# Optimization experiments

Measured on AMD Instinct MI355X. Metric: run time of the kernel, lower is better.

The kernel has to match this reference:

```python
import jax, jax.numpy as jnp
import numpy as np

H = 64          # index_n_heads
D = 128         # index_head_dim (== FP8 quant block size -> one scale per row)
RD = 64         # qk_rope_head_dim
TOPK = 512      # index_topk
THETA = 10000.0
SM_SCALE = D ** -0.5


def _fwht(x):
    """Sylvester-ordered fast Walsh-Hadamard transform over last dim, scaled by d^-0.5."""
    d = x.shape[-1]
    orig = x.shape
    y = x.reshape(-1, d)
    m = 1
    while m < d:  # static loop, log2(d)=7 iters
        y = y.reshape(-1, d // (2 * m), 2, m)
        a, b = y[:, :, 0, :], y[:, :, 1, :]
        y = jnp.stack([a + b, a - b], axis=2)
        m *= 2
    return y.reshape(orig) * (d ** -0.5)


def _interleaved_to_half(x):
    # [..., d] with (even, odd) interleaving -> [evens..., odds...]
    return jnp.concatenate([x[..., 0::2], x[..., 1::2]], axis=-1)


def _rope_half(x, cos, sin):
    # x: [..., RD] in half format; cos/sin broadcastable to [..., RD//2]
    x1, x2 = x[..., : RD // 2], x[..., RD // 2:]
    return jnp.concatenate([x1 * cos - x2 * sin, x2 * cos + x1 * sin], axis=-1)


def _layernorm(x, g, b, eps=1e-5):
    mu = jnp.mean(x, axis=-1, keepdims=True)
    var = jnp.mean(jnp.square(x - mu), axis=-1, keepdims=True)
    return (x - mu) * jax.lax.rsqrt(var + eps) * g + b


def _fp8_ue8m0_quant(x2d):
    """Per-row FP8 e4m3 quantization with UE8M0 (power-of-two) scales. x2d: (M, 128)."""
    amax = jnp.maximum(jnp.max(jnp.abs(x2d), axis=1), 1e-4)
    sf = jnp.exp2(jnp.ceil(jnp.log2(amax / 448.0)))               # (M,)
    xq = (x2d * (1.0 / sf)[:, None]).astype(jnp.float8_e4m3fn)
    return xq, sf


def _indexer_fwd(hidden_states, q_lora, positions, wq_b, wk, w_proj, ln_gamma, ln_beta):
    T = hidden_states.shape[0]
    # --- projections ---
    q = (q_lora @ wq_b).reshape(T, H, D)                          # (T,H,D)
    k = _layernorm(hidden_states @ wk, ln_gamma, ln_beta)         # (T,D)
    # --- RoPE on leading RD dims (interleaved -> half, then half rotation) ---
    inv_freq = 1.0 / (THETA ** (jnp.arange(0, RD, 2, dtype=jnp.float32) / RD))  # (RD/2,)
    ang = positions.astype(jnp.float32)[:, None] * inv_freq       # (T,RD/2)
    cos, sin = jnp.cos(ang), jnp.sin(ang)
    q_rot = _rope_half(_interleaved_to_half(q[..., :RD]), cos[:, None, :], sin[:, None, :])
    k_rot = _rope_half(_interleaved_to_half(k[..., :RD]), cos, sin)
    q = jnp.concatenate([q_rot, q[..., RD:]], axis=-1)
    k = jnp.concatenate([k_rot, k[..., RD:]], axis=-1)
    # --- Hadamard rotation ---
    q = _fwht(q)
    k = _fwht(k)
    # --- FP8 UE8M0 quantization (head_dim == quant block -> 1 scale per row) ---
    q_fp8, q_scale = _fp8_ue8m0_quant(q.reshape(T * H, D))
    k_fp8, k_scale = _fp8_ue8m0_quant(k)
    q_scale = q_scale.reshape(T, H)
    # --- gate weights: weights_proj * H^-0.5 * q_scale * softmax_scale ---
    weights = (hidden_states @ w_proj) * (H ** -0.5) * q_scale * SM_SCALE  # (T,H)
    # --- MQA indexer scoring: dequant matmul, ReLU, head-weighted sum ---
    qd = q_fp8.astype(jnp.float32).reshape(T, H, D)
    kd = k_fp8.astype(jnp.float32) * k_scale[:, None]             # (T,D)
    logits = jnp.einsum('thd,sd->ths', qd, kd)                    # (T,H,S)
    scores = jnp.einsum('th,ths->ts', weights, jax.nn.relu(logits))  # (T,S)
    # --- causal mask + top-k token selection ---
    t_idx = jnp.arange(T)
    causal = t_idx[None, :] <= t_idx[:, None]                     # (T,S): s <= t
    scores = jnp.where(causal, scores, jnp.float32(-1e30))
    vals, idx = jax.lax.top_k(scores, TOPK)
    return vals, idx


def setup_inputs() -> dict:
    key = jax.random.key(0)
    ks = jax.random.split(key, 5)
    T, HID, R = 1024, 7168, 1536
    return {
        'hidden_states': jax.random.normal(ks[0], (T, HID), jnp.float32),
        'q_lora': jax.random.normal(ks[1], (T, R), jnp.float32),
        'positions': jnp.arange(T, dtype=jnp.int32),
        'wq_b': jax.random.normal(ks[2], (R, H * D), jnp.float32) * (R ** -0.5),
        'wk': jax.random.normal(ks[3], (HID, D), jnp.float32) * (HID ** -0.5),
        'w_proj': jax.random.normal(ks[4], (HID, H), jnp.float32) * (HID ** -0.5),
        'ln_gamma': jnp.ones((D,), jnp.float32),
        'ln_beta': jnp.zeros((D,), jnp.float32),
    }


def reference(hidden_states, q_lora, positions, wq_b, wk, w_proj, ln_gamma, ln_beta):
    return _indexer_fwd(hidden_states, q_lora, positions, wq_b, wk, w_proj, ln_gamma, ln_beta)
```

## Files before the change

kernel.cpp:

```cpp
#include <hip/hip_runtime.h>
#include <cstdint>
#include <cmath>

#define NT 1024
#define NHID 7168
#define NR 1536
#define NH 64
#define ND 128
#define NTOPK 512
#define TTILE 4
#define KSPLIT 16

typedef float f32x4 __attribute__((ext_vector_type(4)));
typedef ushort u16x8 __attribute__((ext_vector_type(8)));

__device__ __forceinline__ ushort f2bf(float x) {
  uint32_t u = __float_as_uint(x);
  u += 0x7fffu + ((u >> 16) & 1u);
  return (ushort)(u >> 16);
}
__device__ __forceinline__ float bf2f(ushort u) {
  return __uint_as_float(((uint32_t)u) << 16);
}
__device__ __forceinline__ void gload_lds16(const void* g, void* l) {
  __builtin_amdgcn_global_load_lds(
      (const __attribute__((address_space(1))) uint32_t*)g,
      (__attribute__((address_space(3))) uint32_t*)l, 16, 0, 0);
}
__device__ __forceinline__ uint32_t pk_fp8x4(float a, float b, float c, float d) {
  uint32_t lo = (uint32_t)__builtin_amdgcn_cvt_pk_fp8_f32(a, b, 0, false) & 0xffffu;
  uint32_t hi = (uint32_t)__builtin_amdgcn_cvt_pk_fp8_f32(c, d, 0, false) << 16;
  return lo | hi;
}

__global__ void rope_table_k(const int* __restrict__ pos,
                             float* __restrict__ cost, float* __restrict__ sint) {
  int i = threadIdx.x;
  int t = blockIdx.x;
  if (i < 32) {
    double x = (double)(2 * i) / 64.0;
    double p = pow(10000.0, x);
    float p32 = (float)p;
    float invf = __fdiv_rn(1.0f, p32);
    float ang = __fmul_rn((float)pos[t], invf);
    cost[t * 32 + i] = (float)cos((double)ang);
    sint[t * 32 + i] = (float)sin((double)ang);
  }
}

__global__ __launch_bounds__(256)
void cast_fp8_k(const float* __restrict__ in, uint32_t* __restrict__ out,
                int n8, float scale) {
  int i = blockIdx.x * 256 + threadIdx.x;
  if (i >= n8) return;
  const f32x4* p = (const f32x4*)(in + (size_t)i * 8);
  f32x4 a = p[0], b = p[1];
  out[(size_t)i * 2] =
      pk_fp8x4(a[0] * scale, a[1] * scale, a[2] * scale, a[3] * scale);
  out[(size_t)i * 2 + 1] =
      pk_fp8x4(b[0] * scale, b[1] * scale, b[2] * scale, b[3] * scale);
}

__global__ __launch_bounds__(256)
void tcast_fp8_k(const float* __restrict__ in, uint8_t* __restrict__ out,
                 int K, int N, float scale) {
  __shared__ uint8_t t8[64][68];
  int tid = threadIdx.x;
  int n0 = blockIdx.x * 64, k0 = blockIdx.y * 64;
  int r = tid >> 4, c = (tid & 15) * 4;
#pragma unroll
  for (int rr = 0; rr < 64; rr += 16) {
    f32x4 v = *(const f32x4*)(in + (size_t)(k0 + rr + r) * N + n0 + c);
    *(uint32_t*)&t8[rr + r][c] =
        pk_fp8x4(v[0] * scale, v[1] * scale, v[2] * scale, v[3] * scale);
  }
  __syncthreads();
#pragma unroll
  for (int rr = 0; rr < 64; rr += 16) {
    int orow = rr + r;
    uint32_t w = (uint32_t)t8[c + 0][orow] | ((uint32_t)t8[c + 1][orow] << 8) |
                 ((uint32_t)t8[c + 2][orow] << 16) | ((uint32_t)t8[c + 3][orow] << 24);
    *(uint32_t*)(out + (size_t)(n0 + orow) * K + k0 + c) = w;
  }
}

template <int BM, int BN, bool OUTBF>
__global__ __launch_bounds__(256)
void gemm_fp8_k(const uint8_t* __restrict__ A, const uint8_t* __restrict__ Bt,
                void* __restrict__ Cv, int M, int N, int K, int kchunk) {
  constexpr int FM = BM / 32;
  constexpr int FN = BN / 32;
  __shared__ uint8_t As[2 * BM * 64];
  __shared__ uint8_t Bs[2 * BN * 64];
  int tid = threadIdx.x;
  int wave = tid >> 6, lane = tid & 63;
  int ln = lane & 15, lg = lane >> 4;
  int n0 = blockIdx.x * BN, m0 = blockIdx.y * BM;
  int k0 = blockIdx.z * kchunk;
  int wm = (wave >> 1) * (BM / 2), wn = (wave & 1) * (BN / 2);

  f32x4 acc[FM][FN];
#pragma unroll
  for (int m = 0; m < FM; m++)
#pragma unroll
    for (int n = 0; n < FN; n++) acc[m][n] = {0.f, 0.f, 0.f, 0.f};

  auto stage = [&](int buf, int kk0) {
#pragma unroll
    for (int c = 0; c < BM / 64; c++) {
      int o = c * 256 + wave * 64 + lane;
      int row = o >> 2, g = o & 3;
      int gs = g ^ ((row >> 1) & 3);
      gload_lds16(A + (size_t)(m0 + row) * K + kk0 + gs * 16,
                  (char*)As + buf * (BM * 64) + o * 16);
    }
#pragma unroll
    for (int c = 0; c < BN / 64; c++) {
      int o = c * 256 + wave * 64 + lane;
      int row = o >> 2, g = o & 3;
      int gs = g ^ ((row >> 1) & 3);
      gload_lds16(Bt + (size_t)(n0 + row) * K + kk0 + gs * 16,
                  (char*)Bs + buf * (BN * 64) + o * 16);
    }
  };

  int ntile = kchunk / 64;
  stage(0, k0);
  __syncthreads();
  int cur = 0;
  for (int t = 0; t < ntile; t++) {
    if (t + 1 < ntile) stage(cur ^ 1, k0 + (t + 1) * 64);
    const uint8_t* ap = As + cur * (BM * 64);
    const uint8_t* bp = Bs + cur * (BN * 64);
#pragma unroll
    for (int kk = 0; kk < 2; kk++) {
      long af[FM], bfr[FN];
#pragma unroll
      for (int m = 0; m < FM; m++) {
        int row = wm + m * 16 + ln;
        int g = kk * 2 + (lg >> 1);
        int rd = row * 64 + ((g ^ ((row >> 1) & 3)) << 4) + (lg & 1) * 8;
        af[m] = *(const long*)(ap + rd);
      }
#pragma unroll
      for (int n = 0; n < FN; n++) {
        int row = wn + n * 16 + ln;
        int g = kk * 2 + (lg >> 1);
        int rd = row * 64 + ((g ^ ((row >> 1) & 3)) << 4) + (lg & 1) * 8;
        bfr[n] = *(const long*)(bp + rd);
      }
#pragma unroll
      for (int m = 0; m < FM; m++)
#pragma unroll
        for (int n = 0; n < FN; n++)
          acc[m][n] = __builtin_amdgcn_mfma_f32_16x16x32_fp8_fp8(af[m], bfr[n],
                                                                 acc[m][n], 0, 0, 0);
    }
    __syncthreads();
    cur ^= 1;
  }

  if constexpr (OUTBF) {
    ushort* Cb = (ushort*)Cv;
#pragma unroll
    for (int m = 0; m < FM; m++)
#pragma unroll
      for (int n = 0; n < FN; n++)
#pragma unroll
        for (int j = 0; j < 4; j++) {
          int row = m0 + wm + m * 16 + lg * 4 + j;
          int col = n0 + wn + n * 16 + ln;
          Cb[(size_t)row * N + col] = f2bf(acc[m][n][j]);
        }
  } else {
    float* C = (float*)Cv + (size_t)blockIdx.z * M * N;
#pragma unroll
    for (int m = 0; m < FM; m++)
#pragma unroll
      for (int n = 0; n < FN; n++)
#pragma unroll
        for (int j = 0; j < 4; j++) {
          int row = m0 + wm + m * 16 + lg * 4 + j;
          int col = n0 + wn + n * 16 + ln;
          C[(size_t)row * N + col] = acc[m][n][j];
        }
  }
}

__device__ __forceinline__ void rope_fwht_quant(
    float v0, float v1, int l, int pos_t,
    const float* __restrict__ cost, const float* __restrict__ sint,
    uint8_t* __restrict__ out_bytes, float* __restrict__ out_scale) {
  float a = __shfl(v0, (2 * l) & 63, 64);
  float b = __shfl(v0, (2 * l + 1) & 63, 64);
  int fi = l & 31;
  float c = cost[pos_t * 32 + fi];
  float sn = sint[pos_t * 32 + fi];
  float r;
  if (l < 32)
    r = __fsub_rn(__fmul_rn(a, c), __fmul_rn(b, sn));
  else
    r = __fadd_rn(__fmul_rn(b, c), __fmul_rn(a, sn));
  v0 = r;

#pragma unroll
  for (int m = 1; m < 64; m <<= 1) {
    float p0 = __shfl_xor(v0, m, 64);
    float p1 = __shfl_xor(v1, m, 64);
    bool up = (l & m) == 0;
    v0 = up ? __fadd_rn(v0, p0) : __fsub_rn(p0, v0);
    v1 = up ? __fadd_rn(v1, p1) : __fsub_rn(p1, v1);
  }
  {
    float A0 = v0, B0 = v1;
    v0 = __fadd_rn(A0, B0);
    v1 = __fsub_rn(A0, B0);
  }
  const float WS = 0.08838834764831843f;
  v0 = __fmul_rn(v0, WS);
  v1 = __fmul_rn(v1, WS);

  float am = fmaxf(fabsf(v0), fabsf(v1));
#pragma unroll
  for (int m = 1; m < 64; m <<= 1) am = fmaxf(am, __shfl_xor(am, m, 64));
  am = fmaxf(am, 1e-4f);
  float ratio = __fdiv_rn(am, 448.0f);
  uint32_t rb = __float_as_uint(ratio);
  int e = (int)((rb + 0x7fffffu) >> 23) - 127;
  float sf = __uint_as_float((uint32_t)(e + 127) << 23);
  float inv = __uint_as_float((uint32_t)(127 - e) << 23);
  float q0 = __fmul_rn(v0, inv);
  float q1 = __fmul_rn(v1, inv);
  int b0 = __builtin_amdgcn_cvt_pk_fp8_f32(q0, q0, 0, false);
  int b1 = __builtin_amdgcn_cvt_pk_fp8_f32(q1, q1, 0, false);
  out_bytes[l] = (uint8_t)(b0 & 0xff);
  out_bytes[l + 64] = (uint8_t)(b1 & 0xff);
  if (l == 0) *out_scale = sf;
}

__global__ __launch_bounds__(256)
void kfin_weights_k(const float* __restrict__ kpart, const float* __restrict__ gamma,
                    const float* __restrict__ beta, const float* __restrict__ cost,
                    const float* __restrict__ sint, const float* __restrict__ qscale,
                    uint8_t* __restrict__ kfp8, float* __restrict__ kscale,
                    float* __restrict__ weights) {
  int l = threadIdx.x & 63;
  int row = blockIdx.x * 4 + (threadIdx.x >> 6);
  float v0 = 0.0f, v1 = 0.0f, ws = 0.0f;
#pragma unroll
  for (int p = 0; p < KSPLIT; p++) {
    const float* base = kpart + (size_t)p * (NT * 192) + row * 192;
    v0 = __fadd_rn(v0, base[l]);
    v1 = __fadd_rn(v1, base[l + 64]);
    ws = __fadd_rn(ws, base[128 + l]);
  }
  float w = __fmul_rn(ws, 0.001953125f);
  w = __fmul_rn(w, qscale[row * NH + l]);
  w = __fmul_rn(w, 0.08838834764831843f);
  weights[row * NH + l] = w;
  float s = __fadd_rn(v0, v1);
#pragma unroll
  for (int m = 1; m < 64; m <<= 1) s = __fadd_rn(s, __shfl_xor(s, m, 64));
  float mu = __fmul_rn(s, 0.0078125f);
  float d0 = __fsub_rn(v0, mu), d1 = __fsub_rn(v1, mu);
  float vs = __fadd_rn(__fmul_rn(d0, d0), __fmul_rn(d1, d1));
#pragma unroll
  for (int m = 1; m < 64; m <<= 1) vs = __fadd_rn(vs, __shfl_xor(vs, m, 64));
  float var = __fmul_rn(vs, 0.0078125f);
  float rs = (float)(1.0 / sqrt((double)__fadd_rn(var, 1e-5f)));
  v0 = __fadd_rn(__fmul_rn(__fmul_rn(d0, rs), gamma[l]), beta[l]);
  v1 = __fadd_rn(__fmul_rn(__fmul_rn(d1, rs), gamma[l + 64]), beta[l + 64]);
  rope_fwht_quant(v0, v1, l, row, cost, sint, kfp8 + (size_t)row * ND, kscale + row);
}

__global__ __launch_bounds__(256)
void q_finalize_k(const ushort* __restrict__ qraw, const float* __restrict__ cost,
                  const float* __restrict__ sint, uint8_t* __restrict__ qfp8,
                  float* __restrict__ qscale) {
  int l = threadIdx.x & 63;
  int row = blockIdx.x * 4 + (threadIdx.x >> 6);
  int t = row >> 6;
  float v0 = bf2f(qraw[(size_t)row * ND + l]);
  float v1 = bf2f(qraw[(size_t)row * ND + l + 64]);
  rope_fwht_quant(v0, v1, l, t, cost, sint, qfp8 + (size_t)row * ND, qscale + row);
}

__global__ __launch_bounds__(256)
void scores_k(const uint8_t* __restrict__ qfp8, const uint8_t* __restrict__ kfp8,
              const float* __restrict__ weights, float* __restrict__ scores) {
  __shared__ uint8_t q_lds[TTILE * 64 * 128];
  __shared__ uint8_t k_lds[128 * 128];
  __shared__ float w_lds[TTILE * 64];

  int b = blockIdx.x;
  int g = 0;
  while (g < 7 && b >= 16 * (g + 1) * (g + 2)) g++;
  int r = b - 16 * g * (g + 1);
  int a = 32 * g + r / (g + 1);
  int chunk = r % (g + 1);
  int t0 = a * TTILE;
  int s0 = chunk * 128;

  int tid = threadIdx.x;
  int wave = tid >> 6, lane = tid & 63;
  int lg = lane >> 4, ln = lane & 15;

  const uint8_t* qbase = qfp8 + (size_t)t0 * 64 * 128;
#pragma unroll
  for (int it = 0; it < 8; it++) {
    int o = it * 256 + wave * 64 + lane;
    int row = o >> 3, G = o & 7;
    int src = row * 128 + ((G ^ ((row >> 1) & 7)) << 4);
    gload_lds16(qbase + src, q_lds + (it * 256 + wave * 64) * 16);
  }
  const uint8_t* kbase = kfp8 + (size_t)s0 * 128;
#pragma unroll
  for (int it = 0; it < 4; it++) {
    int o = it * 256 + wave * 64 + lane;
    int row = o >> 3, G = o & 7;
    int src = row * 128 + ((G ^ ((row >> 1) & 7)) << 4);
    gload_lds16(kbase + src, k_lds + (it * 256 + wave * 64) * 16);
  }
  w_lds[tid] = weights[t0 * NH + tid];
  __syncthreads();

  long bfr[2][4];
#pragma unroll
  for (int sj = 0; sj < 2; sj++) {
    int srow = wave * 32 + sj * 16 + ln;
    int base = srow * 128;
    int xr = ((srow >> 1) & 7) << 4;
#pragma unroll
    for (int ks = 0; ks < 4; ks++)
      bfr[sj][ks] = *(const long*)(k_lds + base + ((ks * 32 + lg * 8) ^ xr));
  }

  float p[TTILE][2];
#pragma unroll
  for (int tt = 0; tt < TTILE; tt++) p[tt][0] = p[tt][1] = 0.0f;

#pragma unroll
  for (int ht = 0; ht < 4; ht++) {
    long afr[TTILE][4];
#pragma unroll
    for (int tt = 0; tt < TTILE; tt++) {
      int qrow = tt * 64 + ht * 16 + ln;
      int base = qrow * 128;
      int xr = ((qrow >> 1) & 7) << 4;
#pragma unroll
      for (int ks = 0; ks < 4; ks++)
        afr[tt][ks] = *(const long*)(q_lds + base + ((ks * 32 + lg * 8) ^ xr));
    }
#pragma unroll
    for (int tt = 0; tt < TTILE; tt++) {
      float wj[4];
#pragma unroll
      for (int j = 0; j < 4; j++) wj[j] = w_lds[tt * 64 + ht * 16 + lg * 4 + j];
#pragma unroll
      for (int sj = 0; sj < 2; sj++) {
        f32x4 acc = {0.f, 0.f, 0.f, 0.f};
#pragma unroll
        for (int ks = 0; ks < 4; ks++)
          acc = __builtin_amdgcn_mfma_f32_16x16x32_fp8_fp8(afr[tt][ks], bfr[sj][ks],
                                                           acc, 0, 0, 0);
#pragma unroll
        for (int j = 0; j < 4; j++)
          p[tt][sj] = fmaf(wj[j], fmaxf(acc[j], 0.0f), p[tt][sj]);
      }
    }
  }

#pragma unroll
  for (int tt = 0; tt < TTILE; tt++)
#pragma unroll
    for (int sj = 0; sj < 2; sj++) {
      float v = p[tt][sj];
      v += __shfl_xor(v, 16, 64);
      v += __shfl_xor(v, 32, 64);
      if (lg == 0)
        scores[(size_t)(t0 + tt) * NT + s0 + wave * 32 + sj * 16 + ln] = v;
    }
}

__global__ __launch_bounds__(256)
void topk_k(const float* __restrict__ scores, const float* __restrict__ kscale,
            float* __restrict__ outv, float* __restrict__ outi) {
  __shared__ unsigned long long key[1024];
  int t = blockIdx.x, tid = threadIdx.x;
#pragma unroll
  for (int p = 0; p < 4; p++) {
    int s = tid + p * 256;
    float v;
    if (s <= t) {
      v = __fmul_rn(scores[(size_t)t * NT + s], kscale[s]);
    } else {
      v = -1e30f;
    }
    unsigned u = __float_as_uint(v);
    unsigned ou = (u & 0x80000000u) ? ~u : (u | 0x80000000u);
    key[s] = ((unsigned long long)ou << 32) | (unsigned)(~(unsigned)s);
  }
  for (int k = 2; k <= 1024; k <<= 1) {
    for (int j = k >> 1; j > 0; j >>= 1) {
      __syncthreads();
#pragma unroll
      for (int p = 0; p < 2; p++) {
        int i = tid + p * 256;
        int l = ((i & ~(j - 1)) << 1) | (i & (j - 1));
        int m = l + j;
        bool desc = ((l & k) == 0);
        unsigned long long a = key[l], b = key[m];
        if (desc ? (a < b) : (a > b)) {
          key[l] = b;
          key[m] = a;
        }
      }
    }
  }
  __syncthreads();
#pragma unroll
  for (int p = 0; p < 2; p++) {
    int r = tid + p * 256;
    unsigned long long kk = key[r];
    unsigned ou = (unsigned)(kk >> 32);
    unsigned u = (ou & 0x80000000u) ? (ou ^ 0x80000000u) : ~ou;
    unsigned idx = (~(unsigned)(kk & 0xffffffffu)) & 1023u;
    outv[(size_t)t * NTOPK + r] = __uint_as_float(u);
    outi[(size_t)t * NTOPK + r] = (float)idx;
  }
}

extern "C" void kernel_launch(void* const* d_in, const int* in_sizes, int n_in,
                              void* d_out, int out_size, void* d_ws, size_t ws_size,
                              hipStream_t stream) {
  const float* hidden = (const float*)d_in[0];
  const float* q_lora = (const float*)d_in[1];
  const int* positions = (const int*)d_in[2];
  const float* wq_b = (const float*)d_in[3];
  const float* wk = (const float*)d_in[4];
  const float* w_proj = (const float*)d_in[5];
  const float* ln_g = (const float*)d_in[6];
  const float* ln_b = (const float*)d_in[7];
  float* out = (float*)d_out;

  char* u0 = (char*)d_ws;
  uint8_t* hidden8 = (uint8_t*)u0;
  uint8_t* wkp8 = (uint8_t*)(u0 + 7340032);
  uint8_t* wqb8 = (uint8_t*)u0;
  uint8_t* qlora8 = (uint8_t*)(u0 + 12582912);
  float* scores = (float*)u0;
  char* p = u0 + 14680064;
  ushort* qrawb = (ushort*)p;  p += 16777216;
  float* kpart = (float*)p;    p += 12582912;
  float* cost = (float*)p;     p += 131072;
  float* sint = (float*)p;     p += 131072;
  float* kscale = (float*)p;   p += 4096;
  float* qscale = (float*)p;   p += 262144;
  float* weights = (float*)p;  p += 262144;
  uint8_t* kfp8 = (uint8_t*)p; p += 131072;
  uint8_t* qfp8 = (uint8_t*)p; p += 8388608;

  rope_table_k<<<NT, 64, 0, stream>>>(positions, cost, sint);

  cast_fp8_k<<<NT * NHID / 8 / 256, 256, 0, stream>>>(
      hidden, (uint32_t*)hidden8, NT * NHID / 8, 1.0f);
  tcast_fp8_k<<<dim3(2, 112), 256, 0, stream>>>(wk, wkp8, NHID, ND, 64.0f);
  tcast_fp8_k<<<dim3(1, 112), 256, 0, stream>>>(w_proj, wkp8 + 128 * NHID,
                                                NHID, NH, 64.0f);
  gemm_fp8_k<64, 64, false><<<dim3(3, 16, KSPLIT), 256, 0, stream>>>(
      hidden8, wkp8, kpart, NT, 192, NHID, NHID / KSPLIT);

  cast_fp8_k<<<NT * NR / 8 / 256, 256, 0, stream>>>(
      q_lora, (uint32_t*)qlora8, NT * NR / 8, 1.0f);
  tcast_fp8_k<<<dim3(128, 24), 256, 0, stream>>>(wq_b, wqb8, NR, NH * ND, 1.0f);
  gemm_fp8_k<64, 128, true><<<dim3(64, 16, 1), 256, 0, stream>>>(
      qlora8, wqb8, qrawb, NT, NH * ND, NR, NR);

  q_finalize_k<<<NT * NH / 4, 256, 0, stream>>>(qrawb, cost, sint, qfp8, qscale);
  kfin_weights_k<<<NT / 4, 256, 0, stream>>>(kpart, ln_g, ln_b, cost, sint,
                                             qscale, kfp8, kscale, weights);

  scores_k<<<1152, 256, 0, stream>>>(qfp8, kfp8, weights, scores);
  topk_k<<<NT, 256, 0, stream>>>(scores, kscale, out, out + (size_t)NT * NTOPK);
}
```

Measured before the change: 129.5 us.

## Fuse q RoPE/FWHT/quant into q GEMM epilogue and merge prep kernels

The q projection GEMM now stages its bf16 tile in LDS and performs RoPE, Hadamard transform and FP8 quantization directly, removing the intermediate bf16 q buffer and the separate finalize kernel. The activation casts and RoPE table build are merged into one prep kernel, and the wk/w_proj transposed casts into one launch. This cuts a large global write/read round trip and several launches, at the cost of a serialized per-row epilogue inside the GEMM blocks.

```diff
diff --git a/kernel.cpp b/kernel.cpp
--- a/kernel.cpp
+++ b/kernel.cpp
@@ -12,7 +12,6 @@
 #define KSPLIT 16
 
 typedef float f32x4 __attribute__((ext_vector_type(4)));
-typedef ushort u16x8 __attribute__((ext_vector_type(8)));
 
 __device__ __forceinline__ ushort f2bf(float x) {
   uint32_t u = __float_as_uint(x);
@@ -31,160 +30,6 @@
   uint32_t lo = (uint32_t)__builtin_amdgcn_cvt_pk_fp8_f32(a, b, 0, false) & 0xffffu;
   uint32_t hi = (uint32_t)__builtin_amdgcn_cvt_pk_fp8_f32(c, d, 0, false) << 16;
   return lo | hi;
-}
-
-__global__ void rope_table_k(const int* __restrict__ pos,
-                             float* __restrict__ cost, float* __restrict__ sint) {
-  int i = threadIdx.x;
-  int t = blockIdx.x;
-  if (i < 32) {
-    double x = (double)(2 * i) / 64.0;
-    double p = pow(10000.0, x);
-    float p32 = (float)p;
-    float invf = __fdiv_rn(1.0f, p32);
-    float ang = __fmul_rn((float)pos[t], invf);
-    cost[t * 32 + i] = (float)cos((double)ang);
-    sint[t * 32 + i] = (float)sin((double)ang);
-  }
-}
-
-__global__ __launch_bounds__(256)
-void cast_fp8_k(const float* __restrict__ in, uint32_t* __restrict__ out,
-                int n8, float scale) {
-  int i = blockIdx.x * 256 + threadIdx.x;
-  if (i >= n8) return;
-  const f32x4* p = (const f32x4*)(in + (size_t)i * 8);
-  f32x4 a = p[0], b = p[1];
-  out[(size_t)i * 2] =
-      pk_fp8x4(a[0] * scale, a[1] * scale, a[2] * scale, a[3] * scale);
-  out[(size_t)i * 2 + 1] =
-      pk_fp8x4(b[0] * scale, b[1] * scale, b[2] * scale, b[3] * scale);
-}
-
-__global__ __launch_bounds__(256)
-void tcast_fp8_k(const float* __restrict__ in, uint8_t* __restrict__ out,
-                 int K, int N, float scale) {
-  __shared__ uint8_t t8[64][68];
-  int tid = threadIdx.x;
-  int n0 = blockIdx.x * 64, k0 = blockIdx.y * 64;
-  int r = tid >> 4, c = (tid & 15) * 4;
-#pragma unroll
-  for (int rr = 0; rr < 64; rr += 16) {
-    f32x4 v = *(const f32x4*)(in + (size_t)(k0 + rr + r) * N + n0 + c);
-    *(uint32_t*)&t8[rr + r][c] =
-        pk_fp8x4(v[0] * scale, v[1] * scale, v[2] * scale, v[3] * scale);
-  }
-  __syncthreads();
-#pragma unroll
-  for (int rr = 0; rr < 64; rr += 16) {
-    int orow = rr + r;
-    uint32_t w = (uint32_t)t8[c + 0][orow] | ((uint32_t)t8[c + 1][orow] << 8) |
-                 ((uint32_t)t8[c + 2][orow] << 16) | ((uint32_t)t8[c + 3][orow] << 24);
-    *(uint32_t*)(out + (size_t)(n0 + orow) * K + k0 + c) = w;
-  }
-}
-
-template <int BM, int BN, bool OUTBF>
-__global__ __launch_bounds__(256)
-void gemm_fp8_k(const uint8_t* __restrict__ A, const uint8_t* __restrict__ Bt,
-                void* __restrict__ Cv, int M, int N, int K, int kchunk) {
-  constexpr int FM = BM / 32;
-  constexpr int FN = BN / 32;
-  __shared__ uint8_t As[2 * BM * 64];
-  __shared__ uint8_t Bs[2 * BN * 64];
-  int tid = threadIdx.x;
-  int wave = tid >> 6, lane = tid & 63;
-  int ln = lane & 15, lg = lane >> 4;
-  int n0 = blockIdx.x * BN, m0 = blockIdx.y * BM;
-  int k0 = blockIdx.z * kchunk;
-  int wm = (wave >> 1) * (BM / 2), wn = (wave & 1) * (BN / 2);
-
-  f32x4 acc[FM][FN];
-#pragma unroll
-  for (int m = 0; m < FM; m++)
-#pragma unroll
-    for (int n = 0; n < FN; n++) acc[m][n] = {0.f, 0.f, 0.f, 0.f};
-
-  auto stage = [&](int buf, int kk0) {
-#pragma unroll
-    for (int c = 0; c < BM / 64; c++) {
-      int o = c * 256 + wave * 64 + lane;
-      int row = o >> 2, g = o & 3;
-      int gs = g ^ ((row >> 1) & 3);
-      gload_lds16(A + (size_t)(m0 + row) * K + kk0 + gs * 16,
-                  (char*)As + buf * (BM * 64) + o * 16);
-    }
-#pragma unroll
-    for (int c = 0; c < BN / 64; c++) {
-      int o = c * 256 + wave * 64 + lane;
-      int row = o >> 2, g = o & 3;
-      int gs = g ^ ((row >> 1) & 3);
-      gload_lds16(Bt + (size_t)(n0 + row) * K + kk0 + gs * 16,
-                  (char*)Bs + buf * (BN * 64) + o * 16);
-    }
-  };
-
-  int ntile = kchunk / 64;
-  stage(0, k0);
-  __syncthreads();
-  int cur = 0;
-  for (int t = 0; t < ntile; t++) {
-    if (t + 1 < ntile) stage(cur ^ 1, k0 + (t + 1) * 64);
-    const uint8_t* ap = As + cur * (BM * 64);
-    const uint8_t* bp = Bs + cur * (BN * 64);
-#pragma unroll
-    for (int kk = 0; kk < 2; kk++) {
-      long af[FM], bfr[FN];
-#pragma unroll
-      for (int m = 0; m < FM; m++) {
-        int row = wm + m * 16 + ln;
-        int g = kk * 2 + (lg >> 1);
-        int rd = row * 64 + ((g ^ ((row >> 1) & 3)) << 4) + (lg & 1) * 8;
-        af[m] = *(const long*)(ap + rd);
-      }
-#pragma unroll
-      for (int n = 0; n < FN; n++) {
-        int row = wn + n * 16 + ln;
-        int g = kk * 2 + (lg >> 1);
-        int rd = row * 64 + ((g ^ ((row >> 1) & 3)) << 4) + (lg & 1) * 8;
-        bfr[n] = *(const long*)(bp + rd);
-      }
-#pragma unroll
-      for (int m = 0; m < FM; m++)
-#pragma unroll
-        for (int n = 0; n < FN; n++)
-          acc[m][n] = __builtin_amdgcn_mfma_f32_16x16x32_fp8_fp8(af[m], bfr[n],
-                                                                 acc[m][n], 0, 0, 0);
-    }
-    __syncthreads();
-    cur ^= 1;
-  }
-
-  if constexpr (OUTBF) {
-    ushort* Cb = (ushort*)Cv;
-#pragma unroll
-    for (int m = 0; m < FM; m++)
-#pragma unroll
-      for (int n = 0; n < FN; n++)
-#pragma unroll
-        for (int j = 0; j < 4; j++) {
-          int row = m0 + wm + m * 16 + lg * 4 + j;
-          int col = n0 + wn + n * 16 + ln;
-          Cb[(size_t)row * N + col] = f2bf(acc[m][n][j]);
-        }
-  } else {
-    float* C = (float*)Cv + (size_t)blockIdx.z * M * N;
-#pragma unroll
-    for (int m = 0; m < FM; m++)
-#pragma unroll
-      for (int n = 0; n < FN; n++)
-#pragma unroll
-        for (int j = 0; j < 4; j++) {
-          int row = m0 + wm + m * 16 + lg * 4 + j;
-          int col = n0 + wn + n * 16 + ln;
-          C[(size_t)row * N + col] = acc[m][n][j];
-        }
-  }
 }
 
 __device__ __forceinline__ void rope_fwht_quant(
@@ -239,6 +84,266 @@
 }
 
 __global__ __launch_bounds__(256)
+void prep_k(const float* __restrict__ hidden, const float* __restrict__ q_lora,
+            const int* __restrict__ pos, uint32_t* __restrict__ hidden8,
+            uint32_t* __restrict__ qlora8, float* __restrict__ cost,
+            float* __restrict__ sint) {
+  int gid = blockIdx.x * 256 + threadIdx.x;
+  const int n8h = NT * NHID / 8;
+  if (gid < n8h) {
+    const f32x4* p = (const f32x4*)(hidden + (size_t)gid * 8);
+    f32x4 a = p[0], b = p[1];
+    hidden8[(size_t)gid * 2] = pk_fp8x4(a[0], a[1], a[2], a[3]);
+    hidden8[(size_t)gid * 2 + 1] = pk_fp8x4(b[0], b[1], b[2], b[3]);
+  } else {
+    int i = gid - n8h;
+    const f32x4* p = (const f32x4*)(q_lora + (size_t)i * 8);
+    f32x4 a = p[0], b = p[1];
+    qlora8[(size_t)i * 2] = pk_fp8x4(a[0], a[1], a[2], a[3]);
+    qlora8[(size_t)i * 2 + 1] = pk_fp8x4(b[0], b[1], b[2], b[3]);
+  }
+  if (blockIdx.x < NT && threadIdx.x < 32) {
+    int t = blockIdx.x, i = threadIdx.x;
+    double x = (double)(2 * i) / 64.0;
+    double pw = pow(10000.0, x);
+    float p32 = (float)pw;
+    float invf = __fdiv_rn(1.0f, p32);
+    float ang = __fmul_rn((float)pos[t], invf);
+    cost[t * 32 + i] = (float)cos((double)ang);
+    sint[t * 32 + i] = (float)sin((double)ang);
+  }
+}
+
+__global__ __launch_bounds__(256)
+void tcast_kw_k(const float* __restrict__ wk, const float* __restrict__ wp,
+                uint8_t* __restrict__ out) {
+  __shared__ uint8_t t8[64][68];
+  int tid = threadIdx.x;
+  int bx = blockIdx.x;
+  const float* in = (bx < 2) ? wk : wp;
+  int N = (bx < 2) ? ND : NH;
+  int n0 = (bx < 2) ? bx * 64 : 0;
+  int orow0 = (bx < 2) ? bx * 64 : 128;
+  int k0 = blockIdx.y * 64;
+  int r = tid >> 4, c = (tid & 15) * 4;
+#pragma unroll
+  for (int rr = 0; rr < 64; rr += 16) {
+    f32x4 v = *(const f32x4*)(in + (size_t)(k0 + rr + r) * N + n0 + c);
+    *(uint32_t*)&t8[rr + r][c] =
+        pk_fp8x4(v[0] * 64.0f, v[1] * 64.0f, v[2] * 64.0f, v[3] * 64.0f);
+  }
+  __syncthreads();
+#pragma unroll
+  for (int rr = 0; rr < 64; rr += 16) {
+    int orow = rr + r;
+    uint32_t w = (uint32_t)t8[c + 0][orow] | ((uint32_t)t8[c + 1][orow] << 8) |
+                 ((uint32_t)t8[c + 2][orow] << 16) | ((uint32_t)t8[c + 3][orow] << 24);
+    *(uint32_t*)(out + (size_t)(orow0 + orow) * NHID + k0 + c) = w;
+  }
+}
+
+__global__ __launch_bounds__(256)
+void tcast_fp8_k(const float* __restrict__ in, uint8_t* __restrict__ out,
+                 int K, int N) {
+  __shared__ uint8_t t8[64][68];
+  int tid = threadIdx.x;
+  int n0 = blockIdx.x * 64, k0 = blockIdx.y * 64;
+  int r = tid >> 4, c = (tid & 15) * 4;
+#pragma unroll
+  for (int rr = 0; rr < 64; rr += 16) {
+    f32x4 v = *(const f32x4*)(in + (size_t)(k0 + rr + r) * N + n0 + c);
+    *(uint32_t*)&t8[rr + r][c] = pk_fp8x4(v[0], v[1], v[2], v[3]);
+  }
+  __syncthreads();
+#pragma unroll
+  for (int rr = 0; rr < 64; rr += 16) {
+    int orow = rr + r;
+    uint32_t w = (uint32_t)t8[c + 0][orow] | ((uint32_t)t8[c + 1][orow] << 8) |
+                 ((uint32_t)t8[c + 2][orow] << 16) | ((uint32_t)t8[c + 3][orow] << 24);
+    *(uint32_t*)(out + (size_t)(n0 + orow) * K + k0 + c) = w;
+  }
+}
+
+__global__ __launch_bounds__(256)
+void gemm_kw_k(const uint8_t* __restrict__ A, const uint8_t* __restrict__ Bt,
+               float* __restrict__ C, int M, int N, int K, int kchunk) {
+  __shared__ uint8_t As[2 * 64 * 64];
+  __shared__ uint8_t Bs[2 * 64 * 64];
+  int tid = threadIdx.x;
+  int wave = tid >> 6, lane = tid & 63;
+  int ln = lane & 15, lg = lane >> 4;
+  int n0 = blockIdx.x * 64, m0 = blockIdx.y * 64;
+  int k0 = blockIdx.z * kchunk;
+  int wm = (wave >> 1) * 32, wn = (wave & 1) * 32;
+
+  f32x4 acc[2][2];
+#pragma unroll
+  for (int m = 0; m < 2; m++)
+#pragma unroll
+    for (int n = 0; n < 2; n++) acc[m][n] = {0.f, 0.f, 0.f, 0.f};
+
+  auto stage = [&](int buf, int kk0) {
+    {
+      int o = wave * 64 + lane;
+      int row = o >> 2, g = o & 3;
+      int gs = g ^ ((row >> 1) & 3);
+      gload_lds16(A + (size_t)(m0 + row) * K + kk0 + gs * 16,
+                  (char*)As + buf * 4096 + o * 16);
+    }
+    {
+      int o = wave * 64 + lane;
+      int row = o >> 2, g = o & 3;
+      int gs = g ^ ((row >> 1) & 3);
+      gload_lds16(Bt + (size_t)(n0 + row) * K + kk0 + gs * 16,
+                  (char*)Bs + buf * 4096 + o * 16);
+    }
+  };
+
+  int ntile = kchunk / 64;
+  stage(0, k0);
+  __syncthreads();
+  int cur = 0;
+  for (int t = 0; t < ntile; t++) {
+    if (t + 1 < ntile) stage(cur ^ 1, k0 + (t + 1) * 64);
+    const uint8_t* ap = As + cur * 4096;
+    const uint8_t* bp = Bs + cur * 4096;
+#pragma unroll
+    for (int kk = 0; kk < 2; kk++) {
+      long af[2], bfr[2];
+#pragma unroll
+      for (int m = 0; m < 2; m++) {
+        int row = wm + m * 16 + ln;
+        int g = kk * 2 + (lg >> 1);
+        af[m] = *(const long*)(ap + row * 64 + ((g ^ ((row >> 1) & 3)) << 4) +
+                               (lg & 1) * 8);
+      }
+#pragma unroll
+      for (int n = 0; n < 2; n++) {
+        int row = wn + n * 16 + ln;
+        int g = kk * 2 + (lg >> 1);
+        bfr[n] = *(const long*)(bp + row * 64 + ((g ^ ((row >> 1) & 3)) << 4) +
+                                (lg & 1) * 8);
+      }
+#pragma unroll
+      for (int m = 0; m < 2; m++)
+#pragma unroll
+        for (int n = 0; n < 2; n++)
+          acc[m][n] = __builtin_amdgcn_mfma_f32_16x16x32_fp8_fp8(af[m], bfr[n],
+                                                                 acc[m][n], 0, 0, 0);
+    }
+    __syncthreads();
+    cur ^= 1;
+  }
+
+  float* Cz = C + (size_t)blockIdx.z * M * N;
+#pragma unroll
+  for (int m = 0; m < 2; m++)
+#pragma unroll
+    for (int n = 0; n < 2; n++)
+#pragma unroll
+      for (int j = 0; j < 4; j++) {
+        int row = m0 + wm + m * 16 + lg * 4 + j;
+        int col = n0 + wn + n * 16 + ln;
+        Cz[(size_t)row * N + col] = acc[m][n][j];
+      }
+}
+
+__global__ __launch_bounds__(256)
+void gemm_q_fused_k(const uint8_t* __restrict__ A, const uint8_t* __restrict__ Bt,
+                    const float* __restrict__ cost, const float* __restrict__ sint,
+                    uint8_t* __restrict__ qfp8, float* __restrict__ qscale,
+                    int M, int N, int K) {
+  __shared__ char smem[24576];
+  uint8_t* As = (uint8_t*)smem;
+  uint8_t* Bs = (uint8_t*)smem + 8192;
+  int tid = threadIdx.x;
+  int wave = tid >> 6, lane = tid & 63;
+  int ln = lane & 15, lg = lane >> 4;
+  int n0 = blockIdx.x * 128, m0 = blockIdx.y * 64;
+  int wm = (wave >> 1) * 32, wn = (wave & 1) * 64;
+
+  f32x4 acc[2][4];
+#pragma unroll
+  for (int m = 0; m < 2; m++)
+#pragma unroll
+    for (int n = 0; n < 4; n++) acc[m][n] = {0.f, 0.f, 0.f, 0.f};
+
+  auto stage = [&](int buf, int kk0) {
+    {
+      int o = wave * 64 + lane;
+      int row = o >> 2, g = o & 3;
+      int gs = g ^ ((row >> 1) & 3);
+      gload_lds16(A + (size_t)(m0 + row) * K + kk0 + gs * 16,
+                  (char*)As + buf * 4096 + o * 16);
+    }
+#pragma unroll
+    for (int c = 0; c < 2; c++) {
+      int o = c * 256 + wave * 64 + lane;
+      int row = o >> 2, g = o & 3;
+      int gs = g ^ ((row >> 1) & 3);
+      gload_lds16(Bt + (size_t)(n0 + row) * K + kk0 + gs * 16,
+                  (char*)Bs + buf * 8192 + o * 16);
+    }
+  };
+
+  int ntile = K / 64;
+  stage(0, 0);
+  __syncthreads();
+  int cur = 0;
+  for (int t = 0; t < ntile; t++) {
+    if (t + 1 < ntile) stage(cur ^ 1, (t + 1) * 64);
+    const uint8_t* ap = As + cur * 4096;
+    const uint8_t* bp = Bs + cur * 8192;
+#pragma unroll
+    for (int kk = 0; kk < 2; kk++) {
+      long af[2], bfr[4];
+#pragma unroll
+      for (int m = 0; m < 2; m++) {
+        int row = wm + m * 16 + ln;
+        int g = kk * 2 + (lg >> 1);
+        af[m] = *(const long*)(ap + row * 64 + ((g ^ ((row >> 1) & 3)) << 4) +
+                               (lg & 1) * 8);
+      }
+#pragma unroll
+      for (int n = 0; n < 4; n++) {
+        int row = wn + n * 16 + ln;
+        int g = kk * 2 + (lg >> 1);
+        bfr[n] = *(const long*)(bp + row * 64 + ((g ^ ((row >> 1) & 3)) << 4) +
+                                (lg & 1) * 8);
+      }
+#pragma unroll
+      for (int m = 0; m < 2; m++)
+#pragma unroll
+        for (int n = 0; n < 4; n++)
+          acc[m][n] = __builtin_amdgcn_mfma_f32_16x16x32_fp8_fp8(af[m], bfr[n],
+                                                                 acc[m][n], 0, 0, 0);
+    }
+    __syncthreads();
+    cur ^= 1;
+  }
+
+  ushort(*qtile)[132] = (ushort(*)[132])smem;
+#pragma unroll
+  for (int m = 0; m < 2; m++)
+#pragma unroll
+    for (int n = 0; n < 4; n++)
+#pragma unroll
+      for (int j = 0; j < 4; j++)
+        qtile[wm + m * 16 + lg * 4 + j][wn + n * 16 + ln] = f2bf(acc[m][n][j]);
+  __syncthreads();
+  int h = blockIdx.x;
+  for (int r = 0; r < 16; r++) {
+    int row = wave * 16 + r;
+    int tq = m0 + row;
+    float v0 = bf2f(qtile[row][lane]);
+    float v1 = bf2f(qtile[row][64 + lane]);
+    rope_fwht_quant(v0, v1, lane, tq, cost, sint,
+                    qfp8 + ((size_t)tq * NH + h) * ND,
+                    qscale + (size_t)tq * NH + h);
+  }
+}
+
+__global__ __launch_bounds__(256)
 void kfin_weights_k(const float* __restrict__ kpart, const float* __restrict__ gamma,
                     const float* __restrict__ beta, const float* __restrict__ cost,
                     const float* __restrict__ sint, const float* __restrict__ qscale,
@@ -271,18 +376,6 @@
   v0 = __fadd_rn(__fmul_rn(__fmul_rn(d0, rs), gamma[l]), beta[l]);
   v1 = __fadd_rn(__fmul_rn(__fmul_rn(d1, rs), gamma[l + 64]), beta[l + 64]);
   rope_fwht_quant(v0, v1, l, row, cost, sint, kfp8 + (size_t)row * ND, kscale + row);
-}
-
-__global__ __launch_bounds__(256)
-void q_finalize_k(const ushort* __restrict__ qraw, const float* __restrict__ cost,
-                  const float* __restrict__ sint, uint8_t* __restrict__ qfp8,
-                  float* __restrict__ qscale) {
-  int l = threadIdx.x & 63;
-  int row = blockIdx.x * 4 + (threadIdx.x >> 6);
-  int t = row >> 6;
-  float v0 = bf2f(qraw[(size_t)row * ND + l]);
-  float v1 = bf2f(qraw[(size_t)row * ND + l + 64]);
-  rope_fwht_quant(v0, v1, l, t, cost, sint, qfp8 + (size_t)row * ND, qscale + row);
 }
 
 __global__ __launch_bounds__(256)
@@ -450,7 +543,6 @@
   uint8_t* qlora8 = (uint8_t*)(u0 + 12582912);
   float* scores = (float*)u0;
   char* p = u0 + 14680064;
-  ushort* qrawb = (ushort*)p;  p += 16777216;
   float* kpart = (float*)p;    p += 12582912;
   float* cost = (float*)p;     p += 131072;
   float* sint = (float*)p;     p += 131072;
@@ -460,23 +552,18 @@
   uint8_t* kfp8 = (uint8_t*)p; p += 131072;
   uint8_t* qfp8 = (uint8_t*)p; p += 8388608;
 
-  rope_table_k<<<NT, 64, 0, stream>>>(positions, cost, sint);
-
-  cast_fp8_k<<<NT * NHID / 8 / 256, 256, 0, stream>>>(
-      hidden, (uint32_t*)hidden8, NT * NHID / 8, 1.0f);
-  tcast_fp8_k<<<dim3(2, 112), 256, 0, stream>>>(wk, wkp8, NHID, ND, 64.0f);
-  tcast_fp8_k<<<dim3(1, 112), 256, 0, stream>>>(w_proj, wkp8 + 128 * NHID,
-                                                NHID, NH, 64.0f);
-  gemm_fp8_k<64, 64, false><<<dim3(3, 16, KSPLIT), 256, 0, stream>>>(
+  prep_k<<<(NT * NHID / 8 + NT * NR / 8) / 256, 256, 0, stream>>>(
+      hidden, q_lora, positions, (uint32_t*)hidden8, (uint32_t*)qlora8,
+      cost, sint);
+
+  tcast_kw_k<<<dim3(3, 112), 256, 0, stream>>>(wk, w_proj, wkp8);
+  gemm_kw_k<<<dim3(3, 16, KSPLIT), 256, 0, stream>>>(
       hidden8, wkp8, kpart, NT, 192, NHID, NHID / KSPLIT);
 
-  cast_fp8_k<<<NT * NR / 8 / 256, 256, 0, stream>>>(
-      q_lora, (uint32_t*)qlora8, NT * NR / 8, 1.0f);
-  tcast_fp8_k<<<dim3(128, 24), 256, 0, stream>>>(wq_b, wqb8, NR, NH * ND, 1.0f);
-  gemm_fp8_k<64, 128, true><<<dim3(64, 16, 1), 256, 0, stream>>>(
-      qlora8, wqb8, qrawb, NT, NH * ND, NR, NR);
-
-  q_finalize_k<<<NT * NH / 4, 256, 0, stream>>>(qrawb, cost, sint, qfp8, qscale);
+  tcast_fp8_k<<<dim3(128, 24), 256, 0, stream>>>(wq_b, wqb8, NR, NH * ND);
+  gemm_q_fused_k<<<dim3(64, 16), 256, 0, stream>>>(
+      qlora8, wqb8, cost, sint, qfp8, qscale, NT, NH * ND, NR);
+
   kfin_weights_k<<<NT / 4, 256, 0, stream>>>(kpart, ln_g, ln_b, cost, sint,
                                              qscale, kfp8, kscale, weights);
 
```

Measured after the change: 119.9 us. 1.08x faster.
